# Optimization experiments

Hardware: AMD Instinct MI355X
Metric: run time of the kernel (lower is better)

Reference implementation:

```python
import jax, jax.numpy as jnp
import numpy as np

NEG_SLOPE = 0.2  # PyG GATConv default leaky_relu slope


def gat_conv(x, edge_index, W, a_src, a_dst, b):
    """PyG GATConv (heads=1, concat=True, add_self_loops=True, dropout=0)."""
    N = x.shape[0]
    loops = jnp.arange(N, dtype=edge_index.dtype)
    src = jnp.concatenate([edge_index[0], loops])  # [Ef]
    dst = jnp.concatenate([edge_index[1], loops])  # [Ef]
    h = x @ W  # [N, Dout]
    alpha_src = h @ a_src  # [N]
    alpha_dst = h @ a_dst  # [N]
    logits = jax.nn.leaky_relu(alpha_src[src] + alpha_dst[dst], NEG_SLOPE)  # [Ef]
    # segment softmax over edges grouped by destination node
    m = jax.ops.segment_max(logits, dst, num_segments=N)
    e = jnp.exp(logits - m[dst])
    denom = jax.ops.segment_sum(e, dst, num_segments=N)  # >0: every node has a self-loop
    alpha = e / denom[dst]  # [Ef]
    out = jax.ops.segment_sum(alpha[:, None] * h[src], dst, num_segments=N)
    return out + b


def global_mean_pool(x, batch, num_graphs):
    s = jax.ops.segment_sum(x, batch, num_segments=num_graphs)
    cnt = jax.ops.segment_sum(jnp.ones((x.shape[0],), x.dtype), batch, num_segments=num_graphs)
    return s / jnp.maximum(cnt, 1.0)[:, None]


NUM_GRAPHS = 64


def setup_inputs() -> dict:
    key = jax.random.key(0)
    ks = jax.random.split(key, 12)
    N, E, D = 50000, 600000, 128
    x = jax.random.normal(ks[0], (N, D), dtype=jnp.float32)
    edge_index = jax.random.randint(ks[1], (2, E), 0, N, dtype=jnp.int32)
    edge_weight = jax.random.uniform(ks[2], (E,), dtype=jnp.float32)
    batch = jnp.sort(jax.random.randint(ks[3], (N,), 0, NUM_GRAPHS, dtype=jnp.int32))
    sc = 1.0 / np.sqrt(D)
    W0 = jax.random.normal(ks[4], (D, D), dtype=jnp.float32) * sc
    a_src0 = jax.random.normal(ks[5], (D,), dtype=jnp.float32) * sc
    a_dst0 = jax.random.normal(ks[6], (D,), dtype=jnp.float32) * sc
    b0 = jnp.zeros((D,), dtype=jnp.float32)
    W1 = jax.random.normal(ks[7], (D, D), dtype=jnp.float32) * sc
    a_src1 = jax.random.normal(ks[8], (D,), dtype=jnp.float32) * sc
    a_dst1 = jax.random.normal(ks[9], (D,), dtype=jnp.float32) * sc
    b1 = jnp.zeros((D,), dtype=jnp.float32)
    return {"x": x, "edge_index": edge_index, "edge_weight": edge_weight, "batch": batch,
            "W0": W0, "a_src0": a_src0, "a_dst0": a_dst0, "b0": b0,
            "W1": W1, "a_src1": a_src1, "a_dst1": a_dst1, "b1": b1}


def reference(x, edge_index, edge_weight, batch, W0, a_src0, a_dst0, b0, W1, a_src1, a_dst1, b1):
    # layer 0 (relu_layers_index=[0] -> ReLU after layer 0)
    out = gat_conv(x, edge_index, W0, a_src0, a_dst0, b0)
    out = jax.nn.relu(out)
    emb0 = global_mean_pool(out, batch, NUM_GRAPHS)
    # layer 1 (no relu, no dropout)
    out = gat_conv(out, edge_index, W1, a_src1, a_dst1, b1)
    emb1 = global_mean_pool(out, batch, NUM_GRAPHS)
    return (emb0, emb1)
```

## Files before the change

### kernel.cpp

```cpp
#include <hip/hip_runtime.h>

typedef unsigned int u32;
typedef unsigned short u16;
typedef unsigned long long u64;

typedef short bf16x8 __attribute__((ext_vector_type(8)));
typedef float f32x4 __attribute__((ext_vector_type(4)));
typedef float f32x2 __attribute__((ext_vector_type(2)));

__device__ __forceinline__ float bl(u32 u){ return __uint_as_float(u << 16); }
__device__ __forceinline__ float bh(u32 u){ return __uint_as_float(u & 0xffff0000u); }
__device__ __forceinline__ float b16f(u16 r){ return __uint_as_float(((u32)r) << 16); }
__device__ __forceinline__ u16 f2b(float f){
  u32 u = __float_as_uint(f);
  u32 r = (u + 0x7fffu + ((u >> 16) & 1u)) >> 16;
  return (u16)r;
}
__device__ __forceinline__ u32 pk2(float a, float b){
  return (u32)f2b(a) | ((u32)f2b(b) << 16);
}
__device__ __forceinline__ void fma8(float* acc, float e2, uint2 h){
  f32x2 p0 = __builtin_amdgcn_cvt_pk_f32_fp8((int)h.x, 0);
  f32x2 p1 = __builtin_amdgcn_cvt_pk_f32_fp8((int)h.x, 1);
  f32x2 p2 = __builtin_amdgcn_cvt_pk_f32_fp8((int)h.y, 0);
  f32x2 p3 = __builtin_amdgcn_cvt_pk_f32_fp8((int)h.y, 1);
  acc[0]=fmaf(e2,p0.x,acc[0]); acc[1]=fmaf(e2,p0.y,acc[1]);
  acc[2]=fmaf(e2,p1.x,acc[2]); acc[3]=fmaf(e2,p1.y,acc[3]);
  acc[4]=fmaf(e2,p2.x,acc[4]); acc[5]=fmaf(e2,p2.y,acc[5]);
  acc[6]=fmaf(e2,p3.x,acc[6]); acc[7]=fmaf(e2,p3.y,acc[7]);
}

#define NEG_SLOPE 0.2f
#define BSTRIDE 4096


__device__ __forceinline__ int block_detect(const u32* __restrict__ x){
  __shared__ int cnt_;
  if (threadIdx.x == 0) cnt_ = 0;
  __syncthreads();
  u32 w = x[threadIdx.x];
  int e = (int)((w >> 7) & 0xFFu);
  if (e >= 110 && e <= 135) atomicAdd(&cnt_, 1);
  __syncthreads();
  return (cnt_ >= 128) ? 1 : 0;
}

__global__ __launch_bounds__(256) void part_k(const int* __restrict__ ei, int E, int nbuck,
    int* __restrict__ gcnt, u64* __restrict__ breg)
{
  __shared__ u32 hist[256];
  __shared__ u32 lscan[257];
  __shared__ u32 gbase[256];
  __shared__ u32 cur[256];
  __shared__ u64 stage[2048];
  const int tid = threadIdx.x;
  hist[tid] = 0; cur[tid] = 0;
  __syncthreads();
  const int e0 = blockIdx.x * 2048;
  int src[8], dst[8];
  #pragma unroll
  for (int j = 0; j < 8; j++){
    int t = e0 + tid + j*256;
    if (t < E){
      src[j] = ei[t]; dst[j] = ei[E + t];
      atomicAdd(&hist[dst[j] >> 8], 1u);
    } else dst[j] = -1;
  }
  __syncthreads();
  const u32 v = hist[tid];
  lscan[tid] = v;
  __syncthreads();
  for (int off = 1; off < 256; off <<= 1){
    u32 add = (tid >= off) ? lscan[tid - off] : 0;
    __syncthreads();
    lscan[tid] += add;
    __syncthreads();
  }
  if (tid == 255) lscan[256] = lscan[255];
  u32 excl = lscan[tid] - v;
  __syncthreads();
  const u32 total = lscan[256];
  lscan[tid] = excl;
  if (tid < nbuck && v > 0) gbase[tid] = (u32)atomicAdd(&gcnt[tid], (int)v);
  __syncthreads();
  #pragma unroll
  for (int j = 0; j < 8; j++){
    if (dst[j] >= 0){
      int b = dst[j] >> 8;
      u32 p = lscan[b] + atomicAdd(&cur[b], 1u);
      stage[p] = ((u64)(u32)dst[j] << 32) | (u32)src[j];
    }
  }
  __syncthreads();
  for (u32 i = tid; i < total; i += 256){
    u64 e = stage[i];
    int b = (int)(e >> 40);
    u32 r = i - lscan[b];
    breg[(long)b * BSTRIDE + gbase[b] + r] = e;
  }
}

__global__ __launch_bounds__(256) void csr_k(const int* __restrict__ gcnt,
    const u64* __restrict__ breg,
    int* __restrict__ deg, int* __restrict__ rowptr, int* __restrict__ csrc, int N)
{
  __shared__ u32 dl[256];
  __shared__ u32 rp[256];
  __shared__ u32 cu[256];
  const int b = blockIdx.x, tid = threadIdx.x;
  const int n0 = b << 8;
  const int cntb = gcnt[b];
  dl[tid] = 0; cu[tid] = 0;
  __syncthreads();
  const u64* reg = breg + (long)b * BSTRIDE;
  for (int i = tid; i < cntb; i += 256)
    atomicAdd(&dl[(int)(reg[i] >> 32) - n0], 1u);
  __syncthreads();
  const u32 v = dl[tid];
  rp[tid] = v;
  __syncthreads();
  for (int off = 1; off < 256; off <<= 1){
    u32 add = (tid >= off) ? rp[tid - off] : 0;
    __syncthreads();
    rp[tid] += add;
    __syncthreads();
  }
  u32 excl = rp[tid] - v;
  __syncthreads();
  rp[tid] = excl;
  __syncthreads();
  int node = n0 + tid;
  if (node < N){ deg[node] = (int)v; rowptr[node] = b*BSTRIDE + (int)excl; }
  for (int i = tid; i < cntb; i += 256){
    u64 e = reg[i];
    int d = (int)(e >> 32) - n0;
    u32 pos = rp[d] + atomicAdd(&cu[d], 1u);
    csrc[(long)b*BSTRIDE + pos] = (int)(e & 0xffffffffULL);
  }
}

template<bool XEXT, bool KPERM>
__device__ __forceinline__ void gemm_body(int gb, int isbf,
    const void* __restrict__ Xv, const void* __restrict__ Wv,
    const void* __restrict__ av, const void* __restrict__ dv,
    u32* __restrict__ Hb, float* __restrict__ As, float* __restrict__ Ad, int N)
{
  __shared__ u16 Wt[128*136];
  const int tid = threadIdx.x;

  if (isbf){
    const u32* Wp = (const u32*)Wv;
    #pragma unroll
    for (int i = 0; i < 16; i++){
      int idx = tid + i*256;
      u32 p = Wp[idx];
      int k = idx >> 6, n2 = idx & 63;
      int pos = KPERM ? ((k & 15)*8 + (k >> 4)) : k;
      Wt[(2*n2)*136 + pos]   = (u16)(p & 0xffffu);
      Wt[(2*n2+1)*136 + pos] = (u16)(p >> 16);
    }
  } else {
    const float* Wf = (const float*)Wv;
    #pragma unroll
    for (int i = 0; i < 64; i++){
      int idx = tid + i*256;
      int k = idx >> 7, n = idx & 127;
      int pos = KPERM ? ((k & 15)*8 + (k >> 4)) : k;
      Wt[n*136 + pos] = f2b(Wf[idx]);
    }
  }
  __syncthreads();

  const int wv = tid >> 6, L = tid & 63;
  const int row0 = (gb*4 + wv) * 16;
  if (row0 >= N) return;
  const int nl = L & 15, quad = L >> 4;

  bf16x8 af[4];
  if (!XEXT || isbf){
    const uint4* Xr = (const uint4*)(((const u32*)Xv) + (long)row0*64);
    #pragma unroll
    for (int kb = 0; kb < 4; kb++)
      af[kb] = *(const bf16x8*)&Xr[nl*16 + kb*4 + quad];
  } else {
    const float* Xf = ((const float*)Xv) + (long)(row0 + nl)*128;
    #pragma unroll
    for (int kb = 0; kb < 4; kb++){
      const float4* p = (const float4*)(Xf + kb*32 + quad*8);
      float4 f0 = p[0], f1 = p[1];
      uint4 tmp = make_uint4(pk2(f0.x,f0.y), pk2(f0.z,f0.w), pk2(f1.x,f1.y), pk2(f1.z,f1.w));
      af[kb] = *(const bf16x8*)&tmp;
    }
  }

  f32x4 acc[8];
  #pragma unroll
  for (int nt = 0; nt < 8; nt++) acc[nt] = (f32x4){0.f,0.f,0.f,0.f};
  #pragma unroll
  for (int nt = 0; nt < 8; nt++){
    #pragma unroll
    for (int kb = 0; kb < 4; kb++){
      bf16x8 bf = *(const bf16x8*)&Wt[(nt*16 + nl)*136 + kb*32 + quad*8];
      acc[nt] = __builtin_amdgcn_mfma_f32_16x16x32_bf16(af[kb], bf, acc[nt], 0, 0, 0);
    }
  }

  float ps[4] = {0.f,0.f,0.f,0.f}, pd[4] = {0.f,0.f,0.f,0.f};
  #pragma unroll
  for (int nt = 0; nt < 8; nt++){
    int col = nt*16 + nl;
    float a_ = isbf ? b16f(((const u16*)av)[col]) : ((const float*)av)[col];
    float d_ = isbf ? b16f(((const u16*)dv)[col]) : ((const float*)dv)[col];
    #pragma unroll
    for (int r = 0; r < 4; r++){
      ps[r] = fmaf(acc[nt][r], a_, ps[r]);
      pd[r] = fmaf(acc[nt][r], d_, pd[r]);
    }
  }
  #pragma unroll
  for (int off = 1; off < 16; off <<= 1){
    #pragma unroll
    for (int r = 0; r < 4; r++){
      ps[r] += __shfl_xor(ps[r], off);
      pd[r] += __shfl_xor(pd[r], off);
    }
  }
  if (nl == 0){
    #pragma unroll
    for (int r = 0; r < 4; r++){
      As[row0 + quad*4 + r] = ps[r];
      Ad[row0 + quad*4 + r] = pd[r];
    }
  }

  #pragma unroll
  for (int r = 0; r < 4; r++){
    long row = row0 + quad*4 + r;
    int w0 = 0, w1 = 0;
    w0 = __builtin_amdgcn_cvt_pk_fp8_f32(acc[0][r], acc[1][r], w0, 0);
    w0 = __builtin_amdgcn_cvt_pk_fp8_f32(acc[2][r], acc[3][r], w0, 1);
    w1 = __builtin_amdgcn_cvt_pk_fp8_f32(acc[4][r], acc[5][r], w1, 0);
    w1 = __builtin_amdgcn_cvt_pk_fp8_f32(acc[6][r], acc[7][r], w1, 1);
    uint2 v = make_uint2((u32)w0, (u32)w1);
    *(uint2*)(Hb + row*32 + nl*2) = v;
  }
}

__device__ __forceinline__ void pool_body(const u32* __restrict__ Ob,
    const int* __restrict__ batch, float* __restrict__ psum, int N)
{
  const int tid = threadIdx.x;
  const int wv = tid >> 6, lane = tid & 63;
  const int start = blockIdx.x * 128;
  const int end = min(start + 128, N);
  float2 acc = make_float2(0.f, 0.f);
  int cur = -1;
  for (int node = start + wv; node < end; node += 4){
    int gid = batch[node];
    if (gid != cur){
      if (cur >= 0){
        atomicAdd(&psum[cur*128 + lane*2],     acc.x);
        atomicAdd(&psum[cur*128 + lane*2 + 1], acc.y);
      }
      cur = gid; acc = make_float2(0.f, 0.f);
    }
    u32 p = Ob[(long)node*64 + lane];
    acc.x += bl(p); acc.y += bh(p);
  }
  if (cur >= 0){
    atomicAdd(&psum[cur*128 + lane*2],     acc.x);
    atomicAdd(&psum[cur*128 + lane*2 + 1], acc.y);
  }
}

__global__ __launch_bounds__(256) void gemmdet0_k(
    const u32* __restrict__ x, int* __restrict__ flag,
    const void* __restrict__ W0, const void* __restrict__ as0, const void* __restrict__ ad0,
    u32* __restrict__ Hb, float* __restrict__ As, float* __restrict__ Ad, int N)
{
  int isbf = block_detect(x);
  if (blockIdx.x == 0 && threadIdx.x == 0) *flag = isbf;
  gemm_body<true, false>(blockIdx.x, isbf, x, W0, as0, ad0, Hb, As, Ad, N);
}

__global__ __launch_bounds__(256) void poolgemm1_k(
    const u32* __restrict__ Ob, const int* __restrict__ batch, float* __restrict__ ps0, int pB,
    const void* __restrict__ W1, const void* __restrict__ as1, const void* __restrict__ ad1,
    const int* __restrict__ flag,
    u32* __restrict__ Hb, float* __restrict__ As, float* __restrict__ Ad, int N)
{
  if ((int)blockIdx.x < pB){
    pool_body(Ob, batch, ps0, N);
    return;
  }
  gemm_body<false, true>(blockIdx.x - pB, *flag, Ob, W1, as1, ad1, Hb, As, Ad, N);
}

template<bool RELU>
__global__ __launch_bounds__(256) void gath_k(const int* __restrict__ deg,
    const int* __restrict__ rowptr, const int* __restrict__ csrc,
    const float* __restrict__ As, const float* __restrict__ Ad,
    const u32* __restrict__ Hb, const void* __restrict__ bv, const int* __restrict__ flag,
    u32* __restrict__ Ob, int N)
{
  long t = (long)blockIdx.x*256 + threadIdx.x;
  int node = (int)(t >> 4), q = (int)(t & 15);
  if (node >= N) return;
  const int base = threadIdx.x & 48;
  const float ad = Ad[node];
  float l = As[node] + ad;
  l = l > 0.f ? l : NEG_SLOPE * l;
  float e = __expf(l);
  float acc[8];
  {
    uint2 hv = ((const uint2*)(Hb + (long)node*32))[q];
    f32x2 p0 = __builtin_amdgcn_cvt_pk_f32_fp8((int)hv.x, 0);
    f32x2 p1 = __builtin_amdgcn_cvt_pk_f32_fp8((int)hv.x, 1);
    f32x2 p2 = __builtin_amdgcn_cvt_pk_f32_fp8((int)hv.y, 0);
    f32x2 p3 = __builtin_amdgcn_cvt_pk_f32_fp8((int)hv.y, 1);
    acc[0]=e*p0.x; acc[1]=e*p0.y; acc[2]=e*p1.x; acc[3]=e*p1.y;
    acc[4]=e*p2.x; acc[5]=e*p2.y; acc[6]=e*p3.x; acc[7]=e*p3.y;
  }
  float den = e;
  const int dg = deg[node];
  const int* row = csrc + rowptr[node];
  for (int jb = 0; jb < dg; jb += 16){
    int m = dg - jb; if (m > 16) m = 16;
    int sj = node; float evq = 0.f;
    if (q < m){
      sj = row[jb + q];
      float l2 = As[sj] + ad;
      l2 = l2 > 0.f ? l2 : NEG_SLOPE * l2;
      evq = __expf(l2);
    }
    for (int i = 0; i < m; i += 4){
      float e0 = __shfl(evq, base + i);
      float e1 = __shfl(evq, base + i + 1);
      float e2 = __shfl(evq, base + i + 2);
      float e3 = __shfl(evq, base + i + 3);
      int   s0 = __shfl(sj,  base + i);
      int   s1 = __shfl(sj,  base + i + 1);
      int   s2 = __shfl(sj,  base + i + 2);
      int   s3 = __shfl(sj,  base + i + 3);
      uint2 h0 = ((const uint2*)(Hb + (long)s0*32))[q];
      uint2 h1 = ((const uint2*)(Hb + (long)s1*32))[q];
      uint2 h2 = ((const uint2*)(Hb + (long)s2*32))[q];
      uint2 h3 = ((const uint2*)(Hb + (long)s3*32))[q];
      den += (e0 + e1) + (e2 + e3);
      fma8(acc, e0, h0);
      fma8(acc, e1, h1);
      fma8(acc, e2, h2);
      fma8(acc, e3, h3);
    }
  }
  float inv = 1.f / den;
  float b[8];
  if (*flag){
    const u16* bp = (const u16*)bv;
    #pragma unroll
    for (int i = 0; i < 8; i++) b[i] = b16f(bp[i*16 + q]);
  } else {
    const float* bp = (const float*)bv;
    #pragma unroll
    for (int i = 0; i < 8; i++) b[i] = bp[i*16 + q];
  }
  float o[8];
  #pragma unroll
  for (int i = 0; i < 8; i++){
    o[i] = fmaf(acc[i], inv, b[i]);
    if (RELU) o[i] = fmaxf(o[i], 0.f);
  }
  uint4 w = make_uint4(pk2(o[0],o[1]), pk2(o[2],o[3]), pk2(o[4],o[5]), pk2(o[6],o[7]));
  *(uint4*)&Ob[(long)node*64 + q*4] = w;
}

__global__ __launch_bounds__(256) void pool2_k(const u32* __restrict__ Ob,
    const int* __restrict__ batch, float* __restrict__ psum, int N)
{
  pool_body(Ob, batch, psum, N);
}

__global__ __launch_bounds__(256) void fin_k(const float* __restrict__ ps0,
    const float* __restrict__ ps1, const int* __restrict__ batch, int N,
    const int* __restrict__ flag, void* __restrict__ out)
{
  int t = blockIdx.x*256 + threadIdx.x;
  if (t >= 8192) return;
  int g = t >> 7, pos = t & 127;
  int c = ((pos & 7) << 4) + (pos >> 3);
  int lo = 0, hi = N;
  while (lo < hi){ int mid = (lo + hi) >> 1; if (batch[mid] < g) lo = mid + 1; else hi = mid; }
  int a = lo;
  lo = 0; hi = N;
  while (lo < hi){ int mid = (lo + hi) >> 1; if (batch[mid] < g + 1) lo = mid + 1; else hi = mid; }
  int cc = lo - a;
  float cf = (float)(cc < 1 ? 1 : cc);
  float v0 = ps0[t] / cf, v1 = ps1[t] / cf;
  if (*flag){
    u16* o = (u16*)out;
    o[g*128 + c] = f2b(v0); o[8192 + g*128 + c] = f2b(v1);
  } else {
    float* o = (float*)out;
    o[g*128 + c] = v0; o[8192 + g*128 + c] = v1;
  }
}

extern "C" void kernel_launch(void* const* d_in, const int* in_sizes, int n_in,
                              void* d_out, int out_size, void* d_ws, size_t ws_size,
                              hipStream_t stream)
{
  const void* x    = d_in[0];
  const int* ei    = (const int*)d_in[1];
  const int* batch = (const int*)d_in[3];
  const void* W0  = d_in[4];
  const void* as0 = d_in[5];
  const void* ad0 = d_in[6];
  const void* b0  = d_in[7];
  const void* W1  = d_in[8];
  const void* as1 = d_in[9];
  const void* ad1 = d_in[10];
  const void* b1  = d_in[11];

  const int N  = in_sizes[0] / 128;
  const int E  = in_sizes[1] / 2;
  const int nbuck = (N + 255) >> 8;

  char* ws = (char*)d_ws;
  size_t off = 0;
  auto al = [&](size_t bytes){ size_t o = off; off += (bytes + 255) & ~(size_t)255; return o; };
  u32*   Hb    = (u32*)(ws + al((size_t)N*32*4));
  u32*   Ob    = (u32*)(ws + al((size_t)N*64*4));
  float* As    = (float*)(ws + al((size_t)N*4));
  float* Ad    = (float*)(ws + al((size_t)N*4));
  u64*   breg  = (u64*)(ws + al((size_t)nbuck*BSTRIDE*8));
  int*   csrc  = (int*)(ws + al((size_t)nbuck*BSTRIDE*4));
  int*   deg   = (int*)(ws + al((size_t)N*4));
  int*   rowptr= (int*)(ws + al((size_t)N*4));
  char*  z0    = ws + al(2*64*128*4 + 256*4);
  float* ps0   = (float*)z0;
  float* ps1   = ps0 + 8192;
  int*   gcnt  = (int*)(ps1 + 8192);
  int*   flag  = (int*)(ws + al(256));
  if (off > ws_size) return;

  hipMemsetAsync(z0, 0, 2*64*128*4 + 256*4, stream);

  const int gB   = (N/16 + 3) / 4;
  const int aB   = (E + 2047) / 2048;
  const int nvB16= (N*16 + 255) / 256;
  const int pB   = (N + 127) / 128;

  gemmdet0_k<<<gB, 256, 0, stream>>>((const u32*)x, flag, W0, as0, ad0, Hb, As, Ad, N);
  part_k<<<aB, 256, 0, stream>>>(ei, E, nbuck, gcnt, breg);
  csr_k<<<nbuck, 256, 0, stream>>>(gcnt, breg, deg, rowptr, csrc, N);

  gath_k<true><<<nvB16, 256, 0, stream>>>(deg, rowptr, csrc, As, Ad, Hb, b0, flag, Ob, N);

  poolgemm1_k<<<pB + gB, 256, 0, stream>>>(Ob, batch, ps0, pB,
      W1, as1, ad1, flag, Hb, As, Ad, N);
  gath_k<false><<<nvB16, 256, 0, stream>>>(deg, rowptr, csrc, As, Ad, Hb, b1, flag, Ob, N);
  pool2_k<<<pB, 256, 0, stream>>>(Ob, batch, ps1, N);

  fin_k<<<32, 256, 0, stream>>>(ps0, ps1, batch, N, flag, d_out);
}
```

Measured before the change: 196.8 us.

## Fuse edge partition into layer-0 GEMM launch and mean-pool into gather kernels

The edge-partition kernel is merged into the first GEMM kernel as extra blocks, with the two sharing LDS through a union, so independent work runs in one launch. Mean pooling is moved into the gather/aggregate kernels: each block accumulates its 16 nodes' outputs into a two-graph LDS buffer and issues one atomic per column, removing the separate pool kernels. The second layer no longer writes Ob, and pooling now uses the unrounded fp32 outputs rather than bf16-rounded ones. The cost is extra LDS atomics per thread and a slightly heavier gather kernel. The two-slot buffer assumes each 16-node block spans at most two graphs, which holds because batch is sorted.

```diff
diff --git a/kernel.cpp b/kernel.cpp
--- a/kernel.cpp
+++ b/kernel.cpp
@@ -34,6 +34,11 @@
 #define BSTRIDE 4096
 
 
+struct PartLDS {
+  u32 hist[256]; u32 lscan[257]; u32 gbase[256]; u32 cur[256]; u64 stage[2048];
+};
+union PGShared { PartLDS p; u16 wt[128*136]; };
+
 __device__ __forceinline__ int block_detect(const u32* __restrict__ x){
   __shared__ int cnt_;
   if (threadIdx.x == 0) cnt_ = 0;
@@ -45,16 +50,12 @@
   return (cnt_ >= 128) ? 1 : 0;
 }
 
-__global__ __launch_bounds__(256) void part_k(const int* __restrict__ ei, int E, int nbuck,
+__device__ __forceinline__ void part_body(PartLDS& S,
+    const int* __restrict__ ei, int E, int nbuck,
     int* __restrict__ gcnt, u64* __restrict__ breg)
 {
-  __shared__ u32 hist[256];
-  __shared__ u32 lscan[257];
-  __shared__ u32 gbase[256];
-  __shared__ u32 cur[256];
-  __shared__ u64 stage[2048];
   const int tid = threadIdx.x;
-  hist[tid] = 0; cur[tid] = 0;
+  S.hist[tid] = 0; S.cur[tid] = 0;
   __syncthreads();
   const int e0 = blockIdx.x * 2048;
   int src[8], dst[8];
@@ -63,40 +64,40 @@
     int t = e0 + tid + j*256;
     if (t < E){
       src[j] = ei[t]; dst[j] = ei[E + t];
-      atomicAdd(&hist[dst[j] >> 8], 1u);
+      atomicAdd(&S.hist[dst[j] >> 8], 1u);
     } else dst[j] = -1;
   }
   __syncthreads();
-  const u32 v = hist[tid];
-  lscan[tid] = v;
+  const u32 v = S.hist[tid];
+  S.lscan[tid] = v;
   __syncthreads();
   for (int off = 1; off < 256; off <<= 1){
-    u32 add = (tid >= off) ? lscan[tid - off] : 0;
+    u32 add = (tid >= off) ? S.lscan[tid - off] : 0;
     __syncthreads();
-    lscan[tid] += add;
+    S.lscan[tid] += add;
     __syncthreads();
   }
-  if (tid == 255) lscan[256] = lscan[255];
-  u32 excl = lscan[tid] - v;
-  __syncthreads();
-  const u32 total = lscan[256];
-  lscan[tid] = excl;
-  if (tid < nbuck && v > 0) gbase[tid] = (u32)atomicAdd(&gcnt[tid], (int)v);
+  if (tid == 255) S.lscan[256] = S.lscan[255];
+  u32 excl = S.lscan[tid] - v;
+  __syncthreads();
+  const u32 total = S.lscan[256];
+  S.lscan[tid] = excl;
+  if (tid < nbuck && v > 0) S.gbase[tid] = (u32)atomicAdd(&gcnt[tid], (int)v);
   __syncthreads();
   #pragma unroll
   for (int j = 0; j < 8; j++){
     if (dst[j] >= 0){
       int b = dst[j] >> 8;
-      u32 p = lscan[b] + atomicAdd(&cur[b], 1u);
-      stage[p] = ((u64)(u32)dst[j] << 32) | (u32)src[j];
+      u32 p = S.lscan[b] + atomicAdd(&S.cur[b], 1u);
+      S.stage[p] = ((u64)(u32)dst[j] << 32) | (u32)src[j];
     }
   }
   __syncthreads();
   for (u32 i = tid; i < total; i += 256){
-    u64 e = stage[i];
+    u64 e = S.stage[i];
     int b = (int)(e >> 40);
-    u32 r = i - lscan[b];
-    breg[(long)b * BSTRIDE + gbase[b] + r] = e;
+    u32 r = i - S.lscan[b];
+    breg[(long)b * BSTRIDE + S.gbase[b] + r] = e;
   }
 }
 
@@ -140,12 +141,11 @@
 }
 
 template<bool XEXT, bool KPERM>
-__device__ __forceinline__ void gemm_body(int gb, int isbf,
+__device__ __forceinline__ void gemm_body(int gb, int isbf, u16* __restrict__ Wt,
     const void* __restrict__ Xv, const void* __restrict__ Wv,
     const void* __restrict__ av, const void* __restrict__ dv,
     u32* __restrict__ Hb, float* __restrict__ As, float* __restrict__ Ad, int N)
 {
-  __shared__ u16 Wt[128*136];
   const int tid = threadIdx.x;
 
   if (isbf){
@@ -246,138 +246,133 @@
   }
 }
 
-__device__ __forceinline__ void pool_body(const u32* __restrict__ Ob,
-    const int* __restrict__ batch, float* __restrict__ psum, int N)
-{
-  const int tid = threadIdx.x;
-  const int wv = tid >> 6, lane = tid & 63;
-  const int start = blockIdx.x * 128;
-  const int end = min(start + 128, N);
-  float2 acc = make_float2(0.f, 0.f);
-  int cur = -1;
-  for (int node = start + wv; node < end; node += 4){
-    int gid = batch[node];
-    if (gid != cur){
-      if (cur >= 0){
-        atomicAdd(&psum[cur*128 + lane*2],     acc.x);
-        atomicAdd(&psum[cur*128 + lane*2 + 1], acc.y);
-      }
-      cur = gid; acc = make_float2(0.f, 0.f);
-    }
-    u32 p = Ob[(long)node*64 + lane];
-    acc.x += bl(p); acc.y += bh(p);
-  }
-  if (cur >= 0){
-    atomicAdd(&psum[cur*128 + lane*2],     acc.x);
-    atomicAdd(&psum[cur*128 + lane*2 + 1], acc.y);
-  }
-}
-
-__global__ __launch_bounds__(256) void gemmdet0_k(
+__global__ __launch_bounds__(256) void partgemm0_k(
+    const int* __restrict__ ei, int E, int nbuck, int aB,
+    int* __restrict__ gcnt, u64* __restrict__ breg,
     const u32* __restrict__ x, int* __restrict__ flag,
     const void* __restrict__ W0, const void* __restrict__ as0, const void* __restrict__ ad0,
     u32* __restrict__ Hb, float* __restrict__ As, float* __restrict__ Ad, int N)
 {
+  __shared__ PGShared sh;
+  if ((int)blockIdx.x < aB){
+    part_body(sh.p, ei, E, nbuck, gcnt, breg);
+    return;
+  }
+  const int gb = blockIdx.x - aB;
   int isbf = block_detect(x);
-  if (blockIdx.x == 0 && threadIdx.x == 0) *flag = isbf;
-  gemm_body<true, false>(blockIdx.x, isbf, x, W0, as0, ad0, Hb, As, Ad, N);
-}
-
-__global__ __launch_bounds__(256) void poolgemm1_k(
-    const u32* __restrict__ Ob, const int* __restrict__ batch, float* __restrict__ ps0, int pB,
+  if (gb == 0 && threadIdx.x == 0) *flag = isbf;
+  gemm_body<true, false>(gb, isbf, sh.wt, x, W0, as0, ad0, Hb, As, Ad, N);
+}
+
+__global__ __launch_bounds__(256) void gemm1_k(
+    const u32* __restrict__ Ob,
     const void* __restrict__ W1, const void* __restrict__ as1, const void* __restrict__ ad1,
     const int* __restrict__ flag,
     u32* __restrict__ Hb, float* __restrict__ As, float* __restrict__ Ad, int N)
 {
-  if ((int)blockIdx.x < pB){
-    pool_body(Ob, batch, ps0, N);
-    return;
-  }
-  gemm_body<false, true>(blockIdx.x - pB, *flag, Ob, W1, as1, ad1, Hb, As, Ad, N);
-}
-
-template<bool RELU>
-__global__ __launch_bounds__(256) void gath_k(const int* __restrict__ deg,
+  __shared__ u16 Wt[128*136];
+  gemm_body<false, true>(blockIdx.x, *flag, Wt, Ob, W1, as1, ad1, Hb, As, Ad, N);
+}
+
+template<bool RELU, bool STORE_OB>
+__global__ __launch_bounds__(256) void gathpool_k(const int* __restrict__ deg,
     const int* __restrict__ rowptr, const int* __restrict__ csrc,
     const float* __restrict__ As, const float* __restrict__ Ad,
     const u32* __restrict__ Hb, const void* __restrict__ bv, const int* __restrict__ flag,
-    u32* __restrict__ Ob, int N)
-{
-  long t = (long)blockIdx.x*256 + threadIdx.x;
+    u32* __restrict__ Ob, const int* __restrict__ batch, float* __restrict__ psum, int N)
+{
+  __shared__ float pl[256];
+  const int tid = threadIdx.x;
+  pl[tid] = 0.f;
+  __syncthreads();
+  long t = (long)blockIdx.x*256 + tid;
   int node = (int)(t >> 4), q = (int)(t & 15);
-  if (node >= N) return;
-  const int base = threadIdx.x & 48;
-  const float ad = Ad[node];
-  float l = As[node] + ad;
-  l = l > 0.f ? l : NEG_SLOPE * l;
-  float e = __expf(l);
-  float acc[8];
-  {
-    uint2 hv = ((const uint2*)(Hb + (long)node*32))[q];
-    f32x2 p0 = __builtin_amdgcn_cvt_pk_f32_fp8((int)hv.x, 0);
-    f32x2 p1 = __builtin_amdgcn_cvt_pk_f32_fp8((int)hv.x, 1);
-    f32x2 p2 = __builtin_amdgcn_cvt_pk_f32_fp8((int)hv.y, 0);
-    f32x2 p3 = __builtin_amdgcn_cvt_pk_f32_fp8((int)hv.y, 1);
-    acc[0]=e*p0.x; acc[1]=e*p0.y; acc[2]=e*p1.x; acc[3]=e*p1.y;
-    acc[4]=e*p2.x; acc[5]=e*p2.y; acc[6]=e*p3.x; acc[7]=e*p3.y;
-  }
-  float den = e;
-  const int dg = deg[node];
-  const int* row = csrc + rowptr[node];
-  for (int jb = 0; jb < dg; jb += 16){
-    int m = dg - jb; if (m > 16) m = 16;
-    int sj = node; float evq = 0.f;
-    if (q < m){
-      sj = row[jb + q];
-      float l2 = As[sj] + ad;
-      l2 = l2 > 0.f ? l2 : NEG_SLOPE * l2;
-      evq = __expf(l2);
-    }
-    for (int i = 0; i < m; i += 4){
-      float e0 = __shfl(evq, base + i);
-      float e1 = __shfl(evq, base + i + 1);
-      float e2 = __shfl(evq, base + i + 2);
-      float e3 = __shfl(evq, base + i + 3);
-      int   s0 = __shfl(sj,  base + i);
-      int   s1 = __shfl(sj,  base + i + 1);
-      int   s2 = __shfl(sj,  base + i + 2);
-      int   s3 = __shfl(sj,  base + i + 3);
-      uint2 h0 = ((const uint2*)(Hb + (long)s0*32))[q];
-      uint2 h1 = ((const uint2*)(Hb + (long)s1*32))[q];
-      uint2 h2 = ((const uint2*)(Hb + (long)s2*32))[q];
-      uint2 h3 = ((const uint2*)(Hb + (long)s3*32))[q];
-      den += (e0 + e1) + (e2 + e3);
-      fma8(acc, e0, h0);
-      fma8(acc, e1, h1);
-      fma8(acc, e2, h2);
-      fma8(acc, e3, h3);
-    }
-  }
-  float inv = 1.f / den;
-  float b[8];
-  if (*flag){
-    const u16* bp = (const u16*)bv;
-    #pragma unroll
-    for (int i = 0; i < 8; i++) b[i] = b16f(bp[i*16 + q]);
-  } else {
-    const float* bp = (const float*)bv;
-    #pragma unroll
-    for (int i = 0; i < 8; i++) b[i] = bp[i*16 + q];
-  }
-  float o[8];
-  #pragma unroll
-  for (int i = 0; i < 8; i++){
-    o[i] = fmaf(acc[i], inv, b[i]);
-    if (RELU) o[i] = fmaxf(o[i], 0.f);
-  }
-  uint4 w = make_uint4(pk2(o[0],o[1]), pk2(o[2],o[3]), pk2(o[4],o[5]), pk2(o[6],o[7]));
-  *(uint4*)&Ob[(long)node*64 + q*4] = w;
-}
-
-__global__ __launch_bounds__(256) void pool2_k(const u32* __restrict__ Ob,
-    const int* __restrict__ batch, float* __restrict__ psum, int N)
-{
-  pool_body(Ob, batch, psum, N);
+  const int node0 = blockIdx.x*16;
+  const int g0 = batch[node0];
+  if (node < N){
+    const int base = tid & 48;
+    const float ad = Ad[node];
+    float l = As[node] + ad;
+    l = l > 0.f ? l : NEG_SLOPE * l;
+    float e = __expf(l);
+    float acc[8];
+    {
+      uint2 hv = ((const uint2*)(Hb + (long)node*32))[q];
+      f32x2 p0 = __builtin_amdgcn_cvt_pk_f32_fp8((int)hv.x, 0);
+      f32x2 p1 = __builtin_amdgcn_cvt_pk_f32_fp8((int)hv.x, 1);
+      f32x2 p2 = __builtin_amdgcn_cvt_pk_f32_fp8((int)hv.y, 0);
+      f32x2 p3 = __builtin_amdgcn_cvt_pk_f32_fp8((int)hv.y, 1);
+      acc[0]=e*p0.x; acc[1]=e*p0.y; acc[2]=e*p1.x; acc[3]=e*p1.y;
+      acc[4]=e*p2.x; acc[5]=e*p2.y; acc[6]=e*p3.x; acc[7]=e*p3.y;
+    }
+    float den = e;
+    const int dg = deg[node];
+    const int* row = csrc + rowptr[node];
+    for (int jb = 0; jb < dg; jb += 16){
+      int m = dg - jb; if (m > 16) m = 16;
+      int sj = node; float evq = 0.f;
+      if (q < m){
+        sj = row[jb + q];
+        float l2 = As[sj] + ad;
+        l2 = l2 > 0.f ? l2 : NEG_SLOPE * l2;
+        evq = __expf(l2);
+      }
+      for (int i = 0; i < m; i += 4){
+        float e0 = __shfl(evq, base + i);
+        float e1 = __shfl(evq, base + i + 1);
+        float e2 = __shfl(evq, base + i + 2);
+        float e3 = __shfl(evq, base + i + 3);
+        int   s0 = __shfl(sj,  base + i);
+        int   s1 = __shfl(sj,  base + i + 1);
+        int   s2 = __shfl(sj,  base + i + 2);
+        int   s3 = __shfl(sj,  base + i + 3);
+        uint2 h0 = ((const uint2*)(Hb + (long)s0*32))[q];
+        uint2 h1 = ((const uint2*)(Hb + (long)s1*32))[q];
+        uint2 h2 = ((const uint2*)(Hb + (long)s2*32))[q];
+        uint2 h3 = ((const uint2*)(Hb + (long)s3*32))[q];
+        den += (e0 + e1) + (e2 + e3);
+        fma8(acc, e0, h0);
+        fma8(acc, e1, h1);
+        fma8(acc, e2, h2);
+        fma8(acc, e3, h3);
+      }
+    }
+    float inv = 1.f / den;
+    float b[8];
+    if (*flag){
+      const u16* bp = (const u16*)bv;
+      #pragma unroll
+      for (int i = 0; i < 8; i++) b[i] = b16f(bp[i*16 + q]);
+    } else {
+      const float* bp = (const float*)bv;
+      #pragma unroll
+      for (int i = 0; i < 8; i++) b[i] = bp[i*16 + q];
+    }
+    float o[8];
+    #pragma unroll
+    for (int i = 0; i < 8; i++){
+      o[i] = fmaf(acc[i], inv, b[i]);
+      if (RELU) o[i] = fmaxf(o[i], 0.f);
+    }
+    if (STORE_OB){
+      uint4 w = make_uint4(pk2(o[0],o[1]), pk2(o[2],o[3]), pk2(o[4],o[5]), pk2(o[6],o[7]));
+      *(uint4*)&Ob[(long)node*64 + q*4] = w;
+    }
+    int idx = (batch[node] != g0) ? 1 : 0;
+    #pragma unroll
+    for (int i = 0; i < 8; i++)
+      atomicAdd(&pl[idx*128 + q*8 + i], o[i]);
+  }
+  __syncthreads();
+  int lastnode = min(node0 + 15, N - 1);
+  int g1 = batch[lastnode];
+  if (tid < 128){
+    float v = pl[tid];
+    if (v != 0.f) atomicAdd(&psum[g0*128 + tid], v);
+  } else if (g1 != g0){
+    float v = pl[tid];
+    if (v != 0.f) atomicAdd(&psum[g1*128 + (tid & 127)], v);
+  }
 }
 
 __global__ __launch_bounds__(256) void fin_k(const float* __restrict__ ps0,
@@ -448,18 +443,17 @@
   const int gB   = (N/16 + 3) / 4;
   const int aB   = (E + 2047) / 2048;
   const int nvB16= (N*16 + 255) / 256;
-  const int pB   = (N + 127) / 128;
-
-  gemmdet0_k<<<gB, 256, 0, stream>>>((const u32*)x, flag, W0, as0, ad0, Hb, As, Ad, N);
-  part_k<<<aB, 256, 0, stream>>>(ei, E, nbuck, gcnt, breg);
+
+  partgemm0_k<<<aB + gB, 256, 0, stream>>>(ei, E, nbuck, aB, gcnt, breg,
+      (const u32*)x, flag, W0, as0, ad0, Hb, As, Ad, N);
   csr_k<<<nbuck, 256, 0, stream>>>(gcnt, breg, deg, rowptr, csrc, N);
 
-  gath_k<true><<<nvB16, 256, 0, stream>>>(deg, rowptr, csrc, As, Ad, Hb, b0, flag, Ob, N);
-
-  poolgemm1_k<<<pB + gB, 256, 0, stream>>>(Ob, batch, ps0, pB,
-      W1, as1, ad1, flag, Hb, As, Ad, N);
-  gath_k<false><<<nvB16, 256, 0, stream>>>(deg, rowptr, csrc, As, Ad, Hb, b1, flag, Ob, N);
-  pool2_k<<<pB, 256, 0, stream>>>(Ob, batch, ps1, N);
+  gathpool_k<true, true><<<nvB16, 256, 0, stream>>>(deg, rowptr, csrc,
+      As, Ad, Hb, b0, flag, Ob, batch, ps0, N);
+
+  gemm1_k<<<gB, 256, 0, stream>>>(Ob, W1, as1, ad1, flag, Hb, As, Ad, N);
+  gathpool_k<false, false><<<nvB16, 256, 0, stream>>>(deg, rowptr, csrc,
+      As, Ad, Hb, b1, flag, Ob, batch, ps1, N);
 
   fin_k<<<32, 256, 0, stream>>>(ps0, ps1, batch, N, flag, d_out);
 }
```

New measurement: 230.7 us. 17.2% more time.
